# Kernel tuning notes

Hardware: AMD Instinct MI355X
Metric: run time of the kernel (lower is better)

Reference implementation:

```python
import jax, jax.numpy as jnp
import numpy as np

N_NODES = 20000
N_EDGES = 640000
IN_DIM = 128
HID = 128
NUM_GRAPHS = 64


def setup_inputs() -> dict:
    key = jax.random.key(0)
    ks = jax.random.split(key, 12)
    x = jax.random.normal(ks[0], (N_NODES, IN_DIM), dtype=jnp.float32)
    edge_index = jax.random.randint(ks[1], (2, N_EDGES), 0, N_NODES, dtype=jnp.int64)
    batch = jnp.sort(jax.random.randint(ks[2], (N_NODES,), 0, NUM_GRAPHS, dtype=jnp.int64))
    edge_attr = jax.random.uniform(ks[3], (N_EDGES,), dtype=jnp.float32)
    s1 = 1.0 / np.sqrt(IN_DIM)
    s2 = 1.0 / np.sqrt(HID)
    # GraphConv layer 1: lin_rel (with bias) on aggregated messages, lin_root (no bias) on x
    W1_rel = jax.random.uniform(ks[4], (HID, IN_DIM), minval=-s1, maxval=s1, dtype=jnp.float32)
    b1 = jax.random.uniform(ks[5], (HID,), minval=-s1, maxval=s1, dtype=jnp.float32)
    W1_root = jax.random.uniform(ks[6], (HID, IN_DIM), minval=-s1, maxval=s1, dtype=jnp.float32)
    # GraphConv layer 3 (conv2 is unused in forward)
    W3_rel = jax.random.uniform(ks[7], (HID, HID), minval=-s2, maxval=s2, dtype=jnp.float32)
    b3 = jax.random.uniform(ks[8], (HID,), minval=-s2, maxval=s2, dtype=jnp.float32)
    W3_root = jax.random.uniform(ks[9], (HID, HID), minval=-s2, maxval=s2, dtype=jnp.float32)
    # Final linear head
    Wlin = jax.random.uniform(ks[10], (1, HID), minval=-s2, maxval=s2, dtype=jnp.float32)
    blin = jax.random.uniform(ks[11], (1,), minval=-s2, maxval=s2, dtype=jnp.float32)
    return {
        "x": x, "edge_index": edge_index, "batch": batch, "edge_attr": edge_attr,
        "W1_rel": W1_rel, "b1": b1, "W1_root": W1_root,
        "W3_rel": W3_rel, "b3": b3, "W3_root": W3_root,
        "Wlin": Wlin, "blin": blin, "num_graphs": NUM_GRAPHS,
    }


def graph_conv(x, src, dst, edge_w, W_rel, b_rel, W_root):
    # PyG GraphConv (aggr='add'): out = W_rel @ sum_{j in N(i)} w_ij * x_j + b_rel + W_root @ x_i
    msg = x[src] * edge_w[:, None]                       # [E, d] gather + scale
    agg = jax.ops.segment_sum(msg, dst, num_segments=x.shape[0])  # [N, d] scatter-add
    return agg @ W_rel.T + b_rel + x @ W_root.T


def reference(x, edge_index, batch, edge_attr,
              W1_rel, b1, W1_root, W3_rel, b3, W3_root, Wlin, blin, num_graphs):
    src, dst = edge_index[0], edge_index[1]
    h = graph_conv(x, src, dst, edge_attr, W1_rel, b1, W1_root)
    h = jax.nn.relu(h)
    # dropout p=0.5 is identity in eval mode
    h = graph_conv(h, src, dst, edge_attr, W3_rel, b3, W3_root)
    # global_mean_pool over per-node graph ids
    sums = jax.ops.segment_sum(h, batch, num_segments=num_graphs)          # [G, H]
    counts = jax.ops.segment_sum(jnp.ones((h.shape[0],), h.dtype), batch,
                                 num_segments=num_graphs)                  # [G]
    pooled = sums / jnp.maximum(counts, 1.0)[:, None]
    out = jax.nn.relu(pooled @ Wlin.T + blin)                              # [G, 1]
    return out
```

## Files before the change

### kernel.cpp

```cpp
#include <hip/hip_runtime.h>

#define N_NODES 20000
#define N_EDGES 640000
#define DIM 128
#define NGRAPH 64
#define NBUCK 313
#define EPB 2048
#define NB_GEMM 1252
#define NB_HIST 313
#define RED_BLOCKS 512

__device__ __forceinline__ unsigned int bf16rne(float f) {
    unsigned int u = __float_as_uint(f);
    return (u + 0x7FFFu + ((u >> 16) & 1u)) >> 16;
}

__global__ __launch_bounds__(256, 2) void k_front(
    const float* __restrict__ x, const float* __restrict__ Wrel,
    const float* __restrict__ Wroot, const float* __restrict__ b1,
    unsigned int* __restrict__ yb, float* __restrict__ r,
    const int* __restrict__ dst,
    int* __restrict__ ghist, int* __restrict__ ticket_hist,
    int* __restrict__ boff, int* __restrict__ gcursor,
    const float* __restrict__ W3rel, const float* __restrict__ W3root,
    const float* __restrict__ b3, const float* __restrict__ Wlin,
    float* __restrict__ vrel, float* __restrict__ vroot, float* __restrict__ cb3) {

    __shared__ float sA[64][132];
    __shared__ float sB[64][132];
    __shared__ int lhist[NBUCK];
    __shared__ int islast;

    const int t = threadIdx.x;
    const int blk = blockIdx.x;

    if (blk < NB_GEMM) {
        const int node0 = (blk % 313) * 64;
        const int col0 = (blk / 313) * 64;

        for (int ch = 0; ch < 8; ++ch) {
            int idx = ch * 256 + t;
            int row = idx >> 5;
            int k4 = idx & 31;
            int gn = node0 + row;
            float4 v = make_float4(0.f, 0.f, 0.f, 0.f);
            if (gn < N_NODES) v = ((const float4*)x)[gn * 32 + k4];
            *(float4*)&sA[row][k4 * 4] = v;
        }
        for (int ch = 0; ch < 8; ++ch) {
            int idx = ch * 256 + t;
            int c = idx >> 5;
            int k4 = idx & 31;
            int gc = col0 + c;
            const float* srcw = (gc < DIM) ? (Wrel + gc * DIM) : (Wroot + (gc - DIM) * DIM);
            float4 v = ((const float4*)srcw)[k4];
            int swk = k4 ^ ((c >> 2) & 7);
            *(float4*)&sB[c][swk * 4] = v;
        }
        __syncthreads();

        const int tr = (t >> 4) * 4;
        const int tc = (t & 15) * 4;
        const int u7 = t & 7;
        float acc[4][4] = {};
        for (int k4 = 0; k4 < 32; ++k4) {
            const int k = k4 * 4;
            const int swk = (k4 ^ u7) * 4;
            float4 a[4], b[4];
            for (int i = 0; i < 4; ++i) a[i] = *(const float4*)&sA[tr + i][k];
            for (int j = 0; j < 4; ++j) b[j] = *(const float4*)&sB[tc + j][swk];
            for (int i = 0; i < 4; ++i)
                for (int j = 0; j < 4; ++j)
                    acc[i][j] = fmaf(a[i].x, b[j].x,
                                fmaf(a[i].y, b[j].y,
                                fmaf(a[i].z, b[j].z,
                                fmaf(a[i].w, b[j].w, acc[i][j]))));
        }
        for (int i = 0; i < 4; ++i) {
            int gn = node0 + tr + i;
            if (gn >= N_NODES) continue;
            int gc = col0 + tc;
            if (gc < DIM) {
                uint2 p;
                p.x = bf16rne(acc[i][0]) | (bf16rne(acc[i][1]) << 16);
                p.y = bf16rne(acc[i][2]) | (bf16rne(acc[i][3]) << 16);
                *(uint2*)&yb[gn * 64 + (gc >> 1)] = p;
            } else {
                int c = gc - DIM;
                *(float4*)&r[gn * DIM + c] =
                    make_float4(acc[i][0] + b1[c], acc[i][1] + b1[c + 1],
                                acc[i][2] + b1[c + 2], acc[i][3] + b1[c + 3]);
            }
        }
    } else if (blk < NB_GEMM + NB_HIST) {
        const int hb = blk - NB_GEMM;
        for (int i = t; i < NBUCK; i += 256) lhist[i] = 0;
        __syncthreads();
        const int e0 = hb * EPB;
        for (int i = 0; i < 8; ++i) {
            int e = e0 + i * 256 + t;
            if (e < N_EDGES) atomicAdd(&lhist[dst[e] >> 6], 1);
        }
        __syncthreads();
        for (int i = t; i < NBUCK; i += 256)
            if (lhist[i]) atomicAdd(&ghist[i], lhist[i]);
        __syncthreads();
        if (t == 0) {
            __threadfence();
            int old = atomicAdd(ticket_hist, 1);
            islast = (old == NB_HIST - 1);
        }
        __syncthreads();
        if (islast) {
            __threadfence();
            if (t < 64) {
                int carry = 0;
                for (int c = 0; c < 5; ++c) {
                    int idx = c * 64 + t;
                    int v = (idx < NBUCK)
                        ? __hip_atomic_load(&ghist[idx], __ATOMIC_RELAXED,
                                            __HIP_MEMORY_SCOPE_AGENT)
                        : 0;
                    int xv = v;
                    for (int s = 1; s < 64; s <<= 1) {
                        int u = __shfl_up(xv, s);
                        if (t >= s) xv += u;
                    }
                    int excl = carry + xv - v;
                    if (idx < NBUCK) { boff[idx] = excl; gcursor[idx] = excl; }
                    carry += __shfl(xv, 63);
                }
                if (t == 0) boff[NBUCK] = carry;
            }
        }
    } else {
        if (t < 64) {
            for (int kk = 0; kk < 2; ++kk) {
                int k = t + kk * 64;
                float sr = 0.f, so = 0.f;
                for (int h = 0; h < DIM; ++h) {
                    float wl = Wlin[h];
                    sr = fmaf(wl, W3rel[h * DIM + k], sr);
                    so = fmaf(wl, W3root[h * DIM + k], so);
                }
                vrel[k] = sr;
                vroot[k] = so;
            }
            float c = b3[t] * Wlin[t] + b3[t + 64] * Wlin[t + 64];
            for (int m = 32; m > 0; m >>= 1) c += __shfl_xor(c, m);
            if (t == 0) cb3[0] = c;
        }
    }
}

__global__ __launch_bounds__(256) void k_partition(const int* __restrict__ src,
                                                   const int* __restrict__ dst,
                                                   const float* __restrict__ ew,
                                                   int* __restrict__ gcursor,
                                                   int2* __restrict__ part) {
    __shared__ int lhist[NBUCK], gbase[NBUCK], lcur[NBUCK];
    const int t = threadIdx.x;
    for (int i = t; i < NBUCK; i += 256) lhist[i] = 0;
    __syncthreads();
    const int e0 = blockIdx.x * EPB;
    int mys[8], myd[8];
    float myw[8];
    for (int i = 0; i < 8; ++i) {
        int e = e0 + i * 256 + t;
        if (e < N_EDGES) {
            mys[i] = src[e];
            myd[i] = dst[e];
            myw[i] = ew[e];
            atomicAdd(&lhist[myd[i] >> 6], 1);
        } else {
            myd[i] = -1;
        }
    }
    __syncthreads();
    for (int i = t; i < NBUCK; i += 256) {
        gbase[i] = lhist[i] ? atomicAdd(&gcursor[i], lhist[i]) : 0;
        lcur[i] = 0;
    }
    __syncthreads();
    for (int i = 0; i < 8; ++i) {
        if (myd[i] >= 0) {
            int b = myd[i] >> 6;
            int rk = atomicAdd(&lcur[b], 1);
            part[gbase[b] + rk] =
                make_int2(((myd[i] & 63) << 16) | mys[i], __float_as_int(myw[i]));
        }
    }
}

__global__ __launch_bounds__(256) void k_bucketsort(const int* __restrict__ boff,
                                                    const int2* __restrict__ part,
                                                    int2* __restrict__ sorted,
                                                    int* __restrict__ off) {
    __shared__ int nh[64], ncur[64];
    const int b = blockIdx.x;
    const int t = threadIdx.x;
    const int s0 = boff[b], s1 = boff[b + 1];
    if (t < 64) nh[t] = 0;
    __syncthreads();
    for (int i = s0 + t; i < s1; i += 256) atomicAdd(&nh[part[i].x >> 16], 1);
    __syncthreads();
    if (t < 64) {
        int v = nh[t];
        int xv = v;
        for (int s = 1; s < 64; s <<= 1) {
            int u = __shfl_up(xv, s);
            if (t >= s) xv += u;
        }
        int excl = xv - v;
        ncur[t] = excl;
        int node = b * 64 + t;
        if (node < N_NODES) off[node] = s0 + excl;
    }
    __syncthreads();
    for (int i = s0 + t; i < s1; i += 256) {
        int2 rc = part[i];
        int dl = rc.x >> 16;
        int p = atomicAdd(&ncur[dl], 1);
        sorted[s0 + p] = make_int2(rc.x & 0xFFFF, rc.y);
    }
    if (b == 0 && t == 0) off[N_NODES] = N_EDGES;
}

__global__ __launch_bounds__(256) void k_agg(const unsigned int* __restrict__ yb,
                                             const float2* __restrict__ r2,
                                             const int* __restrict__ off,
                                             const int2* __restrict__ grec,
                                             const float2* __restrict__ vrel2,
                                             const float2* __restrict__ vroot2,
                                             float* __restrict__ aout,
                                             float* __restrict__ bout) {
    const int lane = threadIdx.x & 63;
    const int node = blockIdx.x * 4 + (threadIdx.x >> 6);
    if (node >= N_NODES) return;

    int j = off[node];
    const int e1 = off[node + 1];
    float sx = 0.f, sy = 0.f;
    for (; j + 4 <= e1; j += 4) {
        int2 r0 = grec[j], r1 = grec[j + 1], rr2 = grec[j + 2], r3 = grec[j + 3];
        float w0 = __int_as_float(r0.y), w1 = __int_as_float(r1.y);
        float w2 = __int_as_float(rr2.y), w3 = __int_as_float(r3.y);
        unsigned int v0 = yb[r0.x * 64 + lane];
        unsigned int v1 = yb[r1.x * 64 + lane];
        unsigned int v2 = yb[rr2.x * 64 + lane];
        unsigned int v3 = yb[r3.x * 64 + lane];
        sx = fmaf(w0, __uint_as_float(v0 << 16),
             fmaf(w1, __uint_as_float(v1 << 16),
             fmaf(w2, __uint_as_float(v2 << 16),
             fmaf(w3, __uint_as_float(v3 << 16), sx))));
        sy = fmaf(w0, __uint_as_float(v0 & 0xFFFF0000u),
             fmaf(w1, __uint_as_float(v1 & 0xFFFF0000u),
             fmaf(w2, __uint_as_float(v2 & 0xFFFF0000u),
             fmaf(w3, __uint_as_float(v3 & 0xFFFF0000u), sy))));
    }
    for (; j < e1; ++j) {
        int2 rc = grec[j];
        float w = __int_as_float(rc.y);
        unsigned int v = yb[rc.x * 64 + lane];
        sx = fmaf(w, __uint_as_float(v << 16), sx);
        sy = fmaf(w, __uint_as_float(v & 0xFFFF0000u), sy);
    }
    float2 rr = r2[node * 64 + lane];
    float hx = fmaxf(sx + rr.x, 0.f);
    float hy = fmaxf(sy + rr.y, 0.f);
    float2 vr = vrel2[lane];
    float2 vo = vroot2[lane];
    float pa = hx * vr.x + hy * vr.y;
    float pb = hx * vo.x + hy * vo.y;
    for (int m = 32; m > 0; m >>= 1) {
        pa += __shfl_xor(pa, m);
        pb += __shfl_xor(pb, m);
    }
    if (lane == 0) {
        aout[node] = pa;
        bout[node] = pb;
    }
}

__global__ __launch_bounds__(256) void k_reduce_final(
    const int2* __restrict__ sorted, const int* __restrict__ off,
    const float* __restrict__ a, const float* __restrict__ bvec,
    const int* __restrict__ batch,
    float* __restrict__ gpart, int* __restrict__ gpartc,
    int* __restrict__ ticket_red,
    const float* __restrict__ cb3, const float* __restrict__ blin,
    float* __restrict__ out) {
    __shared__ float sbin[NGRAPH];
    __shared__ int cbin[NGRAPH];
    __shared__ int islast;
    const int t = threadIdx.x;
    for (int i = t; i < NGRAPH; i += 256) { sbin[i] = 0.f; cbin[i] = 0; }
    __syncthreads();
    const int lane = t & 63;
    const int gw = blockIdx.x * 4 + (t >> 6);
    const int nw = gridDim.x * 4;
    for (int node = gw; node < N_NODES; node += nw) {
        const int e0 = off[node], e1 = off[node + 1];
        float s = 0.f;
        for (int j = e0 + lane; j < e1; j += 64) {
            int2 rc = sorted[j];
            s = fmaf(__int_as_float(rc.y), a[rc.x], s);
        }
        for (int m = 32; m > 0; m >>= 1) s += __shfl_xor(s, m);
        if (lane == 0) {
            int g = batch[node];
            atomicAdd(&sbin[g], s + bvec[node]);
            atomicAdd(&cbin[g], 1);
        }
    }
    __syncthreads();
    const int slot = blockIdx.x & 63;
    for (int i = t; i < NGRAPH; i += 256) {
        atomicAdd(&gpart[slot * NGRAPH + i], sbin[i]);
        if (cbin[i]) atomicAdd(&gpartc[slot * NGRAPH + i], cbin[i]);
    }
    __syncthreads();
    if (t == 0) {
        __threadfence();
        islast = (atomicAdd(ticket_red, 1) == (int)gridDim.x - 1);
    }
    __syncthreads();
    if (islast) {
        __threadfence();
        if (t < NGRAPH) {
            float S = 0.f;
            int C = 0;
            for (int s2 = 0; s2 < 64; ++s2) {
                S += __hip_atomic_load(&gpart[s2 * NGRAPH + t], __ATOMIC_RELAXED,
                                       __HIP_MEMORY_SCOPE_AGENT);
                C += __hip_atomic_load(&gpartc[s2 * NGRAPH + t], __ATOMIC_RELAXED,
                                       __HIP_MEMORY_SCOPE_AGENT);
            }
            float denom = (C > 0) ? (float)C : 1.f;
            float v = (S + (float)C * cb3[0]) / denom + blin[0];
            out[t] = (v > 0.f) ? v : 0.f;
        }
    }
}

extern "C" void kernel_launch(void* const* d_in, const int* in_sizes, int n_in,
                              void* d_out, int out_size, void* d_ws, size_t ws_size,
                              hipStream_t stream) {
    const float* x = (const float*)d_in[0];
    const int* edge_index = (const int*)d_in[1];
    const int* src = edge_index;
    const int* dst = edge_index + N_EDGES;
    const int* batch = (const int*)d_in[2];
    const float* ew = (const float*)d_in[3];
    const float* W1rel = (const float*)d_in[4];
    const float* b1 = (const float*)d_in[5];
    const float* W1root = (const float*)d_in[6];
    const float* W3rel = (const float*)d_in[7];
    const float* b3 = (const float*)d_in[8];
    const float* W3root = (const float*)d_in[9];
    const float* Wlin = (const float*)d_in[10];
    const float* blin = (const float*)d_in[11];
    float* out = (float*)d_out;

    char* w = (char*)d_ws;
    size_t o = 0;
    auto alloc = [&](size_t bytes) -> void* {
        void* p = w + o;
        o += bytes;
        o = (o + 255) & ~(size_t)255;
        return p;
    };
    char* zbase = (char*)alloc(1280 + 64 * NGRAPH * 4 * 2);
    int* ghist = (int*)zbase;
    int* ticket_hist = ghist + NBUCK;
    int* ticket_red = ghist + NBUCK + 1;
    float* gpart = (float*)(zbase + 1280);
    int* gpartc = (int*)(zbase + 1280 + 64 * NGRAPH * 4);
    const size_t zbytes = 1280 + 64 * NGRAPH * 4 * 2;

    unsigned int* yb = (unsigned int*)alloc((size_t)N_NODES * DIM * 2);
    float* r = (float*)alloc((size_t)N_NODES * DIM * 4);
    int* boff = (int*)alloc((size_t)(NBUCK + 1) * 4);
    int* gcursor = (int*)alloc((size_t)NBUCK * 4);
    int2* part = (int2*)alloc((size_t)N_EDGES * 8);
    int2* sorted = (int2*)alloc((size_t)N_EDGES * 8);
    int* off = (int*)alloc((size_t)(N_NODES + 1) * 4);
    float* a = (float*)alloc((size_t)N_NODES * 4);
    float* b = (float*)alloc((size_t)N_NODES * 4);
    float* vrel = (float*)alloc(DIM * 4);
    float* vroot = (float*)alloc(DIM * 4);
    float* cb3 = (float*)alloc(4);

    hipMemsetAsync(zbase, 0, zbytes, stream);

    k_front<<<NB_GEMM + NB_HIST + 1, 256, 0, stream>>>(
        x, W1rel, W1root, b1, yb, r, dst, ghist, ticket_hist, boff, gcursor,
        W3rel, W3root, b3, Wlin, vrel, vroot, cb3);

    k_partition<<<NB_HIST, 256, 0, stream>>>(src, dst, ew, gcursor, part);

    k_bucketsort<<<NBUCK, 256, 0, stream>>>(boff, part, sorted, off);

    k_agg<<<(N_NODES + 3) / 4, 256, 0, stream>>>(
        yb, (const float2*)r, off, sorted,
        (const float2*)vrel, (const float2*)vroot, a, b);

    k_reduce_final<<<RED_BLOCKS, 256, 0, stream>>>(
        sorted, off, a, b, batch, gpart, gpartc, ticket_red, cb3, blin, out);
}
```

Measured before the change: 197.5 us.

## Replace FP32 SIMT layer-1 GEMM with split-bf16 MFMA fused into partition kernel

The first layer's dense transform now runs on matrix cores. x and the stacked weights are split into high and low bf16 parts, and three bf16 MFMA products approximate FP32 accuracy. That GEMM moves into a new k_mid kernel that also runs the edge partition blocks, so the two overlap. The cost is extra conversion passes that write bf16 hi/lo copies of x, plus B fragments read straight from global memory and scattered 2-byte output stores.

```diff
diff --git a/kernel.cpp b/kernel.cpp
--- a/kernel.cpp
+++ b/kernel.cpp
@@ -6,94 +6,58 @@
 #define NGRAPH 64
 #define NBUCK 313
 #define EPB 2048
-#define NB_GEMM 1252
+#define NB_CONV 256
 #define NB_HIST 313
+#define NB_WCONV 32
+#define NB_GEMM 313
 #define RED_BLOCKS 512
+
+typedef __attribute__((ext_vector_type(8))) short short8;
+typedef __attribute__((ext_vector_type(4))) float floatx4;
 
 __device__ __forceinline__ unsigned int bf16rne(float f) {
     unsigned int u = __float_as_uint(f);
     return (u + 0x7FFFu + ((u >> 16) & 1u)) >> 16;
 }
 
-__global__ __launch_bounds__(256, 2) void k_front(
-    const float* __restrict__ x, const float* __restrict__ Wrel,
-    const float* __restrict__ Wroot, const float* __restrict__ b1,
-    unsigned int* __restrict__ yb, float* __restrict__ r,
-    const int* __restrict__ dst,
+__global__ __launch_bounds__(256) void k_front(
+    const float* __restrict__ x, const int* __restrict__ dst,
+    const float* __restrict__ Wrel, const float* __restrict__ Wroot,
+    const float* __restrict__ W3rel, const float* __restrict__ W3root,
+    const float* __restrict__ b3, const float* __restrict__ Wlin,
+    unsigned short* __restrict__ xbh, unsigned short* __restrict__ xbl,
+    unsigned short* __restrict__ wbh, unsigned short* __restrict__ wbl,
     int* __restrict__ ghist, int* __restrict__ ticket_hist,
     int* __restrict__ boff, int* __restrict__ gcursor,
-    const float* __restrict__ W3rel, const float* __restrict__ W3root,
-    const float* __restrict__ b3, const float* __restrict__ Wlin,
     float* __restrict__ vrel, float* __restrict__ vroot, float* __restrict__ cb3) {
-
-    __shared__ float sA[64][132];
-    __shared__ float sB[64][132];
-    __shared__ int lhist[NBUCK];
-    __shared__ int islast;
 
     const int t = threadIdx.x;
     const int blk = blockIdx.x;
 
-    if (blk < NB_GEMM) {
-        const int node0 = (blk % 313) * 64;
-        const int col0 = (blk / 313) * 64;
-
-        for (int ch = 0; ch < 8; ++ch) {
-            int idx = ch * 256 + t;
-            int row = idx >> 5;
-            int k4 = idx & 31;
-            int gn = node0 + row;
-            float4 v = make_float4(0.f, 0.f, 0.f, 0.f);
-            if (gn < N_NODES) v = ((const float4*)x)[gn * 32 + k4];
-            *(float4*)&sA[row][k4 * 4] = v;
-        }
-        for (int ch = 0; ch < 8; ++ch) {
-            int idx = ch * 256 + t;
-            int c = idx >> 5;
-            int k4 = idx & 31;
-            int gc = col0 + c;
-            const float* srcw = (gc < DIM) ? (Wrel + gc * DIM) : (Wroot + (gc - DIM) * DIM);
-            float4 v = ((const float4*)srcw)[k4];
-            int swk = k4 ^ ((c >> 2) & 7);
-            *(float4*)&sB[c][swk * 4] = v;
-        }
-        __syncthreads();
-
-        const int tr = (t >> 4) * 4;
-        const int tc = (t & 15) * 4;
-        const int u7 = t & 7;
-        float acc[4][4] = {};
-        for (int k4 = 0; k4 < 32; ++k4) {
-            const int k = k4 * 4;
-            const int swk = (k4 ^ u7) * 4;
-            float4 a[4], b[4];
-            for (int i = 0; i < 4; ++i) a[i] = *(const float4*)&sA[tr + i][k];
-            for (int j = 0; j < 4; ++j) b[j] = *(const float4*)&sB[tc + j][swk];
-            for (int i = 0; i < 4; ++i)
-                for (int j = 0; j < 4; ++j)
-                    acc[i][j] = fmaf(a[i].x, b[j].x,
-                                fmaf(a[i].y, b[j].y,
-                                fmaf(a[i].z, b[j].z,
-                                fmaf(a[i].w, b[j].w, acc[i][j]))));
-        }
-        for (int i = 0; i < 4; ++i) {
-            int gn = node0 + tr + i;
-            if (gn >= N_NODES) continue;
-            int gc = col0 + tc;
-            if (gc < DIM) {
-                uint2 p;
-                p.x = bf16rne(acc[i][0]) | (bf16rne(acc[i][1]) << 16);
-                p.y = bf16rne(acc[i][2]) | (bf16rne(acc[i][3]) << 16);
-                *(uint2*)&yb[gn * 64 + (gc >> 1)] = p;
-            } else {
-                int c = gc - DIM;
-                *(float4*)&r[gn * DIM + c] =
-                    make_float4(acc[i][0] + b1[c], acc[i][1] + b1[c + 1],
-                                acc[i][2] + b1[c + 2], acc[i][3] + b1[c + 3]);
-            }
-        }
-    } else if (blk < NB_GEMM + NB_HIST) {
-        const int hb = blk - NB_GEMM;
+    if (blk < NB_CONV) {
+        const float4* x4 = (const float4*)x;
+        uint2* xh2 = (uint2*)xbh;
+        uint2* xl2 = (uint2*)xbl;
+        for (int i = blk * 256 + t; i < N_NODES * 32; i += NB_CONV * 256) {
+            float4 v = x4[i];
+            unsigned int h0 = bf16rne(v.x), h1 = bf16rne(v.y);
+            unsigned int h2 = bf16rne(v.z), h3 = bf16rne(v.w);
+            float l0 = v.x - __uint_as_float(h0 << 16);
+            float l1 = v.y - __uint_as_float(h1 << 16);
+            float l2 = v.z - __uint_as_float(h2 << 16);
+            float l3 = v.w - __uint_as_float(h3 << 16);
+            uint2 hp, lp;
+            hp.x = h0 | (h1 << 16);
+            hp.y = h2 | (h3 << 16);
+            lp.x = bf16rne(l0) | (bf16rne(l1) << 16);
+            lp.y = bf16rne(l2) | (bf16rne(l3) << 16);
+            xh2[i] = hp;
+            xl2[i] = lp;
+        }
+    } else if (blk < NB_CONV + NB_HIST) {
+        __shared__ int lhist[NBUCK];
+        __shared__ int islast;
+        const int hb = blk - NB_CONV;
         for (int i = t; i < NBUCK; i += 256) lhist[i] = 0;
         __syncthreads();
         const int e0 = hb * EPB;
@@ -107,8 +71,7 @@
         __syncthreads();
         if (t == 0) {
             __threadfence();
-            int old = atomicAdd(ticket_hist, 1);
-            islast = (old == NB_HIST - 1);
+            islast = (atomicAdd(ticket_hist, 1) == NB_HIST - 1);
         }
         __syncthreads();
         if (islast) {
@@ -133,6 +96,15 @@
                 if (t == 0) boff[NBUCK] = carry;
             }
         }
+    } else if (blk < NB_CONV + NB_HIST + NB_WCONV) {
+        const int b = blk - (NB_CONV + NB_HIST);
+        for (int i = b * 256 + t; i < 256 * DIM; i += NB_WCONV * 256) {
+            int n = i >> 7, k = i & 127;
+            float v = (n < DIM) ? Wrel[n * DIM + k] : Wroot[(n - DIM) * DIM + k];
+            unsigned int h = bf16rne(v);
+            wbh[i] = (unsigned short)h;
+            wbl[i] = (unsigned short)bf16rne(v - __uint_as_float(h << 16));
+        }
     } else {
         if (t < 64) {
             for (int kk = 0; kk < 2; ++kk) {
@@ -153,41 +125,95 @@
     }
 }
 
-__global__ __launch_bounds__(256) void k_partition(const int* __restrict__ src,
-                                                   const int* __restrict__ dst,
-                                                   const float* __restrict__ ew,
-                                                   int* __restrict__ gcursor,
-                                                   int2* __restrict__ part) {
-    __shared__ int lhist[NBUCK], gbase[NBUCK], lcur[NBUCK];
+__global__ __launch_bounds__(256) void k_mid(
+    const int* __restrict__ src, const int* __restrict__ dst,
+    const float* __restrict__ ew,
+    int* __restrict__ gcursor, int2* __restrict__ part,
+    const unsigned short* __restrict__ xbh, const unsigned short* __restrict__ xbl,
+    const unsigned short* __restrict__ wbh, const unsigned short* __restrict__ wbl,
+    const float* __restrict__ b1,
+    unsigned short* __restrict__ yb, float* __restrict__ r) {
+
     const int t = threadIdx.x;
-    for (int i = t; i < NBUCK; i += 256) lhist[i] = 0;
-    __syncthreads();
-    const int e0 = blockIdx.x * EPB;
-    int mys[8], myd[8];
-    float myw[8];
-    for (int i = 0; i < 8; ++i) {
-        int e = e0 + i * 256 + t;
-        if (e < N_EDGES) {
-            mys[i] = src[e];
-            myd[i] = dst[e];
-            myw[i] = ew[e];
-            atomicAdd(&lhist[myd[i] >> 6], 1);
-        } else {
-            myd[i] = -1;
-        }
-    }
-    __syncthreads();
-    for (int i = t; i < NBUCK; i += 256) {
-        gbase[i] = lhist[i] ? atomicAdd(&gcursor[i], lhist[i]) : 0;
-        lcur[i] = 0;
-    }
-    __syncthreads();
-    for (int i = 0; i < 8; ++i) {
-        if (myd[i] >= 0) {
-            int b = myd[i] >> 6;
-            int rk = atomicAdd(&lcur[b], 1);
-            part[gbase[b] + rk] =
-                make_int2(((myd[i] & 63) << 16) | mys[i], __float_as_int(myw[i]));
+    if (blockIdx.x < NB_HIST) {
+        __shared__ int lhist[NBUCK], gbase[NBUCK], lcur[NBUCK];
+        for (int i = t; i < NBUCK; i += 256) lhist[i] = 0;
+        __syncthreads();
+        const int e0 = blockIdx.x * EPB;
+        int mys[8], myd[8];
+        float myw[8];
+        for (int i = 0; i < 8; ++i) {
+            int e = e0 + i * 256 + t;
+            if (e < N_EDGES) {
+                mys[i] = src[e];
+                myd[i] = dst[e];
+                myw[i] = ew[e];
+                atomicAdd(&lhist[myd[i] >> 6], 1);
+            } else {
+                myd[i] = -1;
+            }
+        }
+        __syncthreads();
+        for (int i = t; i < NBUCK; i += 256) {
+            gbase[i] = lhist[i] ? atomicAdd(&gcursor[i], lhist[i]) : 0;
+            lcur[i] = 0;
+        }
+        __syncthreads();
+        for (int i = 0; i < 8; ++i) {
+            if (myd[i] >= 0) {
+                int b = myd[i] >> 6;
+                int rk = atomicAdd(&lcur[b], 1);
+                part[gbase[b] + rk] =
+                    make_int2(((myd[i] & 63) << 16) | mys[i], __float_as_int(myw[i]));
+            }
+        }
+    } else {
+        const int g = blockIdx.x - NB_HIST;
+        const int lane = t & 63;
+        const int m = lane & 15;
+        const int q = lane >> 4;
+        const int row0 = g * 64 + (t >> 6) * 16;
+
+        const short8* Ah = (const short8*)xbh;
+        const short8* Al = (const short8*)xbl;
+        const short8* Bh = (const short8*)wbh;
+        const short8* Bl = (const short8*)wbl;
+        const int arow = (row0 + m) * 16 + q;
+
+        floatx4 acc[16];
+        #pragma unroll
+        for (int i = 0; i < 16; ++i) acc[i] = (floatx4)(0.f);
+
+        #pragma unroll
+        for (int kc = 0; kc < 4; ++kc) {
+            short8 ah = Ah[arow + kc * 4];
+            short8 al = Al[arow + kc * 4];
+            #pragma unroll
+            for (int nt = 0; nt < 16; ++nt) {
+                int bidx = (nt * 16 + m) * 16 + kc * 4 + q;
+                short8 bh = Bh[bidx];
+                short8 bl = Bl[bidx];
+                acc[nt] = __builtin_amdgcn_mfma_f32_16x16x32_bf16(ah, bh, acc[nt], 0, 0, 0);
+                acc[nt] = __builtin_amdgcn_mfma_f32_16x16x32_bf16(al, bh, acc[nt], 0, 0, 0);
+                acc[nt] = __builtin_amdgcn_mfma_f32_16x16x32_bf16(ah, bl, acc[nt], 0, 0, 0);
+            }
+        }
+
+        #pragma unroll
+        for (int nt = 0; nt < 16; ++nt) {
+            int col = nt * 16 + m;
+            float bias = (col >= DIM) ? b1[col - DIM] : 0.f;
+            #pragma unroll
+            for (int reg = 0; reg < 4; ++reg) {
+                int row = row0 + q * 4 + reg;
+                if (row < N_NODES) {
+                    float v = acc[nt][reg];
+                    if (col < DIM)
+                        yb[row * DIM + col] = (unsigned short)bf16rne(v);
+                    else
+                        r[row * DIM + (col - DIM)] = v + bias;
+                }
+            }
         }
     }
 }
@@ -272,9 +298,9 @@
     float2 vo = vroot2[lane];
     float pa = hx * vr.x + hy * vr.y;
     float pb = hx * vo.x + hy * vo.y;
-    for (int m = 32; m > 0; m >>= 1) {
-        pa += __shfl_xor(pa, m);
-        pb += __shfl_xor(pb, m);
+    for (int mm = 32; mm > 0; mm >>= 1) {
+        pa += __shfl_xor(pa, mm);
+        pb += __shfl_xor(pb, mm);
     }
     if (lane == 0) {
         aout[node] = pa;
@@ -306,7 +332,7 @@
             int2 rc = sorted[j];
             s = fmaf(__int_as_float(rc.y), a[rc.x], s);
         }
-        for (int m = 32; m > 0; m >>= 1) s += __shfl_xor(s, m);
+        for (int mm = 32; mm > 0; mm >>= 1) s += __shfl_xor(s, mm);
         if (lane == 0) {
             int g = batch[node];
             atomicAdd(&sbin[g], s + bvec[node]);
@@ -378,7 +404,11 @@
     int* gpartc = (int*)(zbase + 1280 + 64 * NGRAPH * 4);
     const size_t zbytes = 1280 + 64 * NGRAPH * 4 * 2;
 
-    unsigned int* yb = (unsigned int*)alloc((size_t)N_NODES * DIM * 2);
+    unsigned short* xbh = (unsigned short*)alloc((size_t)20032 * DIM * 2);
+    unsigned short* xbl = (unsigned short*)alloc((size_t)20032 * DIM * 2);
+    unsigned short* wbh = (unsigned short*)alloc((size_t)256 * DIM * 2);
+    unsigned short* wbl = (unsigned short*)alloc((size_t)256 * DIM * 2);
+    unsigned short* yb = (unsigned short*)alloc((size_t)N_NODES * DIM * 2);
     float* r = (float*)alloc((size_t)N_NODES * DIM * 4);
     int* boff = (int*)alloc((size_t)(NBUCK + 1) * 4);
     int* gcursor = (int*)alloc((size_t)NBUCK * 4);
@@ -393,16 +423,18 @@
 
     hipMemsetAsync(zbase, 0, zbytes, stream);
 
-    k_front<<<NB_GEMM + NB_HIST + 1, 256, 0, stream>>>(
-        x, W1rel, W1root, b1, yb, r, dst, ghist, ticket_hist, boff, gcursor,
-        W3rel, W3root, b3, Wlin, vrel, vroot, cb3);
-
-    k_partition<<<NB_HIST, 256, 0, stream>>>(src, dst, ew, gcursor, part);
+    k_front<<<NB_CONV + NB_HIST + NB_WCONV + 1, 256, 0, stream>>>(
+        x, dst, W1rel, W1root, W3rel, W3root, b3, Wlin,
+        xbh, xbl, wbh, wbl, ghist, ticket_hist, boff, gcursor,
+        vrel, vroot, cb3);
+
+    k_mid<<<NB_HIST + NB_GEMM, 256, 0, stream>>>(
+        src, dst, ew, gcursor, part, xbh, xbl, wbh, wbl, b1, yb, r);
 
     k_bucketsort<<<NBUCK, 256, 0, stream>>>(boff, part, sorted, off);
 
     k_agg<<<(N_NODES + 3) / 4, 256, 0, stream>>>(
-        yb, (const float2*)r, off, sorted,
+        (const unsigned int*)yb, (const float2*)r, off, sorted,
         (const float2*)vrel, (const float2*)vroot, a, b);
 
     k_reduce_final<<<RED_BLOCKS, 256, 0, stream>>>(
```

Measured after the change: 207.1 us. 4.9% more time.
